# Kernel tuning notes

Hardware: AMD Instinct MI355X
Metric: run time of the kernel (lower is better)

The kernel has to match this reference:

```python
import jax, jax.numpy as jnp
import numpy as np

NUM_HEADER = 8
DIM_HIDDEN = 512
DIM_HEADER = DIM_HIDDEN // NUM_HEADER


def setup_inputs() -> dict:
    key = jax.random.key(0)
    ks = jax.random.split(key, 11)
    B, S, D = 2, 4096, DIM_HIDDEN
    scale = 1.0 / np.sqrt(D)
    inp = {
        "q": jax.random.normal(ks[0], (B, S, D), jnp.float32),
        "k": jax.random.normal(ks[1], (B, S, D), jnp.float32),
        "v": jax.random.normal(ks[2], (B, S, D), jnp.float32),
        # nn.Linear weights are [out, in]; y = x @ W.T + b
        "Wq": jax.random.normal(ks[3], (D, D), jnp.float32) * scale,
        "bq": jax.random.normal(ks[4], (D,), jnp.float32) * scale,
        "Wk": jax.random.normal(ks[5], (D, D), jnp.float32) * scale,
        "bk": jax.random.normal(ks[6], (D,), jnp.float32) * scale,
        "Wv": jax.random.normal(ks[7], (D, D), jnp.float32) * scale,
        "bv": jax.random.normal(ks[8], (D,), jnp.float32) * scale,
        "Wo": jax.random.normal(ks[9], (D, D), jnp.float32) * scale,
        "bo": jax.random.normal(ks[10], (D,), jnp.float32) * scale,
    }
    return inp


def reference(q, k, v, Wq, bq, Wk, bk, Wv, bv, Wo, bo):
    B = q.shape[0]
    H, dh = NUM_HEADER, DIM_HEADER

    def proj(x, W, b):
        # [B,S,D] -> [B,H,S,dh]
        y = jnp.einsum('bsd,ed->bse', x, W) + b
        return y.reshape(B, -1, H, dh).transpose(0, 2, 1, 3)

    qh = proj(q, Wq, bq)
    kh = proj(k, Wk, bk)
    vh = proj(v, Wv, bv)

    scores = jnp.einsum('bhqd,bhkd->bhqk', qh, kh) / jnp.sqrt(jnp.float32(dh))
    attn = jax.nn.softmax(scores, axis=-1)
    ctx = jnp.einsum('bhqk,bhkd->bhqd', attn, vh)
    concat = ctx.transpose(0, 2, 1, 3).reshape(B, -1, H * dh)
    return jnp.einsum('bsd,ed->bse', concat, Wo) + bo
```

## Files before the change

kernel.cpp:

```cpp
#include <hip/hip_runtime.h>
#include <hip/hip_bf16.h>

typedef __attribute__((ext_vector_type(8))) short short8;
typedef __attribute__((ext_vector_type(4))) float f32x4;
typedef __attribute__((ext_vector_type(16))) float f32x16;
typedef __attribute__((ext_vector_type(4))) float f4v;

#define SEQ 4096
#define NBH 16
#define SCALE_Q 0.18033688011112042f
#define CSHIFT 16.0f

#define MFMA16(a, b, c) __builtin_amdgcn_mfma_f32_16x16x32_bf16(a, b, c, 0, 0, 0)
#define MFMA32(a, b, c) __builtin_amdgcn_mfma_f32_32x32x16_bf16(a, b, c, 0, 0, 0)

__device__ __forceinline__ short f2bf(float f) {
  union { float f; unsigned u; } x; x.f = f;
  unsigned r = x.u + 0x7FFFu + ((x.u >> 16) & 1u);
  return (short)(r >> 16);
}

__device__ __forceinline__ unsigned cvt_pk_bf16(float lo, float hi) {
  unsigned r;
  asm("v_cvt_pk_bf16_f32 %0, %1, %2" : "=v"(r) : "v"(lo), "v"(hi));
  return r;
}

__device__ __forceinline__ short8 cvt8(const float* __restrict__ src) {
  f4v v0 = *(const f4v*)src;
  f4v v1 = *(const f4v*)(src + 4);
  union { unsigned u[4]; short8 s; } r;
  r.u[0] = cvt_pk_bf16(v0[0], v0[1]);
  r.u[1] = cvt_pk_bf16(v0[2], v0[3]);
  r.u[2] = cvt_pk_bf16(v1[0], v1[1]);
  r.u[3] = cvt_pk_bf16(v1[2], v1[3]);
  return r.s;
}

__device__ __forceinline__ void gll16(const void* g, void* l) {
  __builtin_amdgcn_global_load_lds(
      (const __attribute__((address_space(1))) void*)g,
      (__attribute__((address_space(3))) void*)l, 16, 0, 0);
}

__device__ __forceinline__ void pswap(unsigned& a, unsigned& b) {
  asm volatile("v_permlane32_swap_b32 %0, %1" : "+v"(a), "+v"(b));
}

__global__ __launch_bounds__(256) void cvt_w(
    const float* __restrict__ w0, const float* __restrict__ w1,
    const float* __restrict__ w2, const float* __restrict__ w3,
    short* __restrict__ dst)
{
  int i = blockIdx.x * 256 + threadIdx.x;
  int m = i >> 15;
  int off = (i & 32767) * 8;
  const float* s = (m == 0) ? w0 : (m == 1) ? w1 : (m == 2) ? w2 : w3;
  *(short8*)(dst + (size_t)m * 262144 + off) = cvt8(s + off);
}

template <int MODE>
__global__ __launch_bounds__(256) void gemm_bt(
    const float* __restrict__ Af, const short* __restrict__ Ab,
    const short* __restrict__ Wb, const float* __restrict__ bias,
    void* __restrict__ Cout)
{
  __shared__ __align__(16) char smemA[64 * 72 * 2];
  __shared__ __align__(16) char smemB[128 * 64 * 2];
  short (*As)[72] = (short(*)[72])smemA;
  const int t    = threadIdx.x;
  const int lane = t & 63;
  const int w    = t >> 6;
  const int g    = lane >> 4;
  const int q    = lane & 15;
  const int tile_n = blockIdx.x * 128;
  const int tile_m = blockIdx.y * 64;

  f32x4 acc[4][2];
#pragma unroll
  for (int mi = 0; mi < 4; ++mi)
#pragma unroll
    for (int ni = 0; ni < 2; ++ni)
#pragma unroll
      for (int j = 0; j < 4; ++j) acc[mi][ni][j] = 0.f;

  for (int k0 = 0; k0 < 512; k0 += 64) {
    __syncthreads();
    if (MODE != 3) {
#pragma unroll
      for (int it = 0; it < 2; ++it) {
        int i = it * 256 + t;
        int r = i >> 3, sg = i & 7;
        *(short8*)&As[r][sg * 8] =
            cvt8(Af + (size_t)(tile_m + r) * 512 + k0 + sg * 8);
      }
    } else {
#pragma unroll
      for (int it = 0; it < 2; ++it) {
        int i = it * 256 + t;
        int row = i >> 3, cg = i & 7;
        const char* gp = (const char*)Ab +
            ((size_t)(tile_m + row) * 512 + k0) * 2 + ((cg ^ (row & 7)) << 4);
        gll16(gp, smemA + (size_t)(it * 256 + (t & ~63)) * 16);
      }
    }
#pragma unroll
    for (int it = 0; it < 4; ++it) {
      int i = it * 256 + t;
      int row = i >> 3, cg = i & 7;
      const char* gp = (const char*)Wb +
          ((size_t)(tile_n + row) * 512 + k0) * 2 + ((cg ^ (row & 7)) << 4);
      gll16(gp, smemB + (size_t)(it * 256 + (t & ~63)) * 16);
    }
    __syncthreads();
#pragma unroll
    for (int kk = 0; kk < 2; ++kk) {
      short8 af[4], bfv[2];
#pragma unroll
      for (int mi = 0; mi < 4; ++mi) {
        int rA = mi * 16 + q;
        if (MODE != 3)
          af[mi] = *(const short8*)&As[rA][kk * 32 + g * 8];
        else
          af[mi] = *(const short8*)(smemA + rA * 128 +
                                    (((4 * kk + g) ^ (rA & 7)) << 4));
      }
#pragma unroll
      for (int ni = 0; ni < 2; ++ni) {
        int rB = w * 32 + ni * 16 + q;
        bfv[ni] = *(const short8*)(smemB + rB * 128 +
                                   (((4 * kk + g) ^ (rB & 7)) << 4));
      }
#pragma unroll
      for (int mi = 0; mi < 4; ++mi)
#pragma unroll
        for (int ni = 0; ni < 2; ++ni) {
          if (MODE == 2)
            acc[mi][ni] = MFMA16(bfv[ni], af[mi], acc[mi][ni]);
          else
            acc[mi][ni] = MFMA16(af[mi], bfv[ni], acc[mi][ni]);
        }
    }
  }

#pragma unroll
  for (int mi = 0; mi < 4; ++mi) {
#pragma unroll
    for (int ni = 0; ni < 2; ++ni) {
#pragma unroll
      for (int j = 0; j < 4; ++j) {
        if (MODE == 2) {
          int e = tile_n + w * 32 + ni * 16 + 4 * g + j;
          int srow = tile_m + mi * 16 + q;
          float val = acc[mi][ni][j] + bias[e];
          int b = srow >> 12, sl = srow & 4095;
          int h = e >> 6, d = e & 63;
          ((short*)Cout)[((size_t)((b * 8 + h) * 64 + d)) * SEQ + sl] = f2bf(val);
        } else {
          int m = tile_m + mi * 16 + g * 4 + j;
          int e = tile_n + w * 32 + ni * 16 + q;
          float val = acc[mi][ni][j] + bias[e];
          if (MODE == 0) val *= SCALE_Q;
          if (MODE == 3) {
            ((float*)Cout)[(size_t)m * 512 + e] = val;
          } else {
            int b = m >> 12, s = m & 4095;
            int h = e >> 6, d = e & 63;
            ((short*)Cout)[((size_t)(b * 8 + h) * SEQ + s) * 64 + d] = f2bf(val);
          }
        }
      }
    }
  }
}

template <int NSPLIT>
__global__ __launch_bounds__(256, 4) void attn_kernel(
    const short* __restrict__ Qh, const short* __restrict__ Kh,
    const short* __restrict__ Vt, short* __restrict__ ctx,
    float* __restrict__ Opart, float* __restrict__ lsum)
{
  __shared__ __align__(16) char smem[2][16384];
  const int t    = threadIdx.x;
  const int lane = t & 63;
  const int w    = t >> 6;
  const int l31  = lane & 31;
  const int hi   = lane >> 5;

  const int fid = blockIdx.x;
  int qt, bh, split;
  if (NSPLIT == 1) {
    int lid = (fid & 7) * 64 + (fid >> 3);
    qt = lid & 31; bh = lid >> 5; split = 0;
  } else {
    int lid = (fid & 7) * 128 + (fid >> 3);
    qt = lid & 31; split = (lid >> 5) & 1; bh = lid >> 6;
  }
  const int NT  = (SEQ / 64) / NSPLIT;
  const int kt0 = split * NT;

  const size_t kbase = (size_t)bh * SEQ * 64;
  const size_t vbase = (size_t)bh * 64 * SEQ;
  const int q0 = qt * 128 + w * 32;

  short8 qf[4];
#pragma unroll
  for (int m = 0; m < 4; ++m)
    qf[m] = *(const short8*)(Qh + kbase + (size_t)(q0 + l31) * 64 + m * 16 + hi * 8);

  f32x16 fz, fm;
#pragma unroll
  for (int r = 0; r < 16; ++r) { fz[r] = 0.f; fm[r] = -CSHIFT; }
  f32x16 acc0 = fz, acc1 = fz;
  float lrun = 0.f;

  const int rif  = lane >> 3;
  const int scol = ((lane & 7) ^ rif) * 16;
  const int xr   = (hi * 16) ^ ((lane & 7) << 4);

#define STAGE(buf, kt)                                                         \
  {                                                                            \
    _Pragma("unroll")                                                          \
    for (int i = 0; i < 4; ++i) {                                              \
      int c = w * 4 + i;                                                       \
      char* ldst = &smem[buf][c * 1024];                                       \
      if (c < 8) {                                                             \
        int row = c * 8 + rif;                                                 \
        const char* gp = (const char*)Kh +                                     \
            ((kbase + (size_t)((kt) * 64 + row) * 64) * 2 + scol);             \
        gll16(gp, ldst);                                                       \
      } else {                                                                 \
        int row = (c - 8) * 8 + rif;                                           \
        const char* gp = (const char*)Vt +                                     \
            ((vbase + (size_t)row * SEQ + (kt) * 64) * 2 + scol);              \
        gll16(gp, ldst);                                                       \
      }                                                                        \
    }                                                                          \
  }

  STAGE(0, kt0);
  int cur = 0;

  for (int it = 0; it < NT; ++it) {
    const int kt = kt0 + it;
    if (it < NT - 1) {
      STAGE(cur ^ 1, kt + 1);
      asm volatile("s_waitcnt vmcnt(4)" ::: "memory");
    } else {
      asm volatile("s_waitcnt vmcnt(0)" ::: "memory");
    }
    __builtin_amdgcn_sched_barrier(0);
    __builtin_amdgcn_s_barrier();
    __builtin_amdgcn_sched_barrier(0);

    const char* Kb = &smem[cur][0];
    const char* Vb = &smem[cur][8192];

    f32x16 s0, s1;
    {
      short8 k0 = *(const short8*)(Kb + (size_t)(l31) * 128 + ((32 * 0) ^ xr));
      short8 k1 = *(const short8*)(Kb + (size_t)(32 + l31) * 128 + ((32 * 0) ^ xr));
      __builtin_amdgcn_s_setprio(1);
      s0 = MFMA32(k0, qf[0], fm);
      s1 = MFMA32(k1, qf[0], fm);
      __builtin_amdgcn_s_setprio(0);
    }
#pragma unroll
    for (int m = 1; m < 4; ++m) {
      short8 k0 = *(const short8*)(Kb + (size_t)(l31) * 128 + ((32 * m) ^ xr));
      short8 k1 = *(const short8*)(Kb + (size_t)(32 + l31) * 128 + ((32 * m) ^ xr));
      __builtin_amdgcn_s_setprio(1);
      s0 = MFMA32(k0, qf[m], s0);
      s1 = MFMA32(k1, qf[m], s1);
      __builtin_amdgcn_s_setprio(0);
    }

#pragma unroll
    for (int r = 0; r < 16; ++r) s0[r] = __builtin_amdgcn_exp2f(s0[r]);
    float rs0;
    {
      float b_[8];
#pragma unroll
      for (int r = 0; r < 8; ++r) b_[r] = s0[r] + s0[r + 8];
#pragma unroll
      for (int r = 0; r < 4; ++r) b_[r] += b_[r + 4];
      rs0 = (b_[0] + b_[1]) + (b_[2] + b_[3]);
    }
    union { unsigned u[4]; short8 v; } A0c, A1c;
    {
      unsigned p0 = cvt_pk_bf16(s0[0], s0[1]);
      unsigned p1 = cvt_pk_bf16(s0[2], s0[3]);
      unsigned p2 = cvt_pk_bf16(s0[4], s0[5]);
      unsigned p3 = cvt_pk_bf16(s0[6], s0[7]);
      unsigned p4 = cvt_pk_bf16(s0[8], s0[9]);
      unsigned p5 = cvt_pk_bf16(s0[10], s0[11]);
      unsigned p6 = cvt_pk_bf16(s0[12], s0[13]);
      unsigned p7 = cvt_pk_bf16(s0[14], s0[15]);
      pswap(p0, p2); pswap(p1, p3); pswap(p4, p6); pswap(p5, p7);
      A0c.u[0] = p0; A0c.u[1] = p1; A0c.u[2] = p2; A0c.u[3] = p3;
      A1c.u[0] = p4; A1c.u[1] = p5; A1c.u[2] = p6; A1c.u[3] = p7;
    }
#pragma unroll
    for (int h2 = 0; h2 < 2; ++h2) {
      short8 pa = h2 ? A1c.v : A0c.v;
      short8 vf0 = *(const short8*)(Vb + (size_t)(l31) * 128 + ((32 * h2) ^ xr));
      short8 vf1 = *(const short8*)(Vb + (size_t)(32 + l31) * 128 + ((32 * h2) ^ xr));
      __builtin_amdgcn_s_setprio(1);
      acc0 = MFMA32(pa, vf0, acc0);
      acc1 = MFMA32(pa, vf1, acc1);
      __builtin_amdgcn_s_setprio(0);
    }

#pragma unroll
    for (int r = 0; r < 16; ++r) s1[r] = __builtin_amdgcn_exp2f(s1[r]);
    float rs1;
    {
      float b_[8];
#pragma unroll
      for (int r = 0; r < 8; ++r) b_[r] = s1[r] + s1[r + 8];
#pragma unroll
      for (int r = 0; r < 4; ++r) b_[r] += b_[r + 4];
      rs1 = (b_[0] + b_[1]) + (b_[2] + b_[3]);
    }
    {
      unsigned p0 = cvt_pk_bf16(s1[0], s1[1]);
      unsigned p1 = cvt_pk_bf16(s1[2], s1[3]);
      unsigned p2 = cvt_pk_bf16(s1[4], s1[5]);
      unsigned p3 = cvt_pk_bf16(s1[6], s1[7]);
      unsigned p4 = cvt_pk_bf16(s1[8], s1[9]);
      unsigned p5 = cvt_pk_bf16(s1[10], s1[11]);
      unsigned p6 = cvt_pk_bf16(s1[12], s1[13]);
      unsigned p7 = cvt_pk_bf16(s1[14], s1[15]);
      pswap(p0, p2); pswap(p1, p3); pswap(p4, p6); pswap(p5, p7);
      A0c.u[0] = p0; A0c.u[1] = p1; A0c.u[2] = p2; A0c.u[3] = p3;
      A1c.u[0] = p4; A1c.u[1] = p5; A1c.u[2] = p6; A1c.u[3] = p7;
    }
#pragma unroll
    for (int h2 = 0; h2 < 2; ++h2) {
      short8 pa = h2 ? A1c.v : A0c.v;
      short8 vf0 = *(const short8*)(Vb + (size_t)(l31) * 128 + ((64 + 32 * h2) ^ xr));
      short8 vf1 = *(const short8*)(Vb + (size_t)(32 + l31) * 128 + ((64 + 32 * h2) ^ xr));
      __builtin_amdgcn_s_setprio(1);
      acc0 = MFMA32(pa, vf0, acc0);
      acc1 = MFMA32(pa, vf1, acc1);
      __builtin_amdgcn_s_setprio(0);
    }

    float rs = rs0 + rs1;
    rs += __shfl_xor(rs, 32);
    lrun += rs;

    __builtin_amdgcn_sched_barrier(0);
    __builtin_amdgcn_s_barrier();
    __builtin_amdgcn_sched_barrier(0);
    cur ^= 1;
  }

  if (NSPLIT == 1) {
    const int b = bh >> 3, hh = bh & 7;
    const float inv = 1.0f / lrun;
#pragma unroll
    for (int r = 0; r < 16; ++r) {
      int ql = (r & 3) + 8 * (r >> 2) + 4 * hi;
      float iv = __shfl(inv, ql);
      int qrow = q0 + ql;
      size_t off = ((size_t)(b * SEQ + qrow)) * 512 + hh * 64 + l31;
      ctx[off]      = f2bf(acc0[r] * iv);
      ctx[off + 32] = f2bf(acc1[r] * iv);
    }
  } else {
    float* Ob = Opart + (((size_t)(split * NBH + bh) * SEQ + q0)) * 64;
#pragma unroll
    for (int r = 0; r < 16; ++r) {
      int ql = (r & 3) + 8 * (r >> 2) + 4 * hi;
      Ob[(size_t)ql * 64 + l31]      = acc0[r];
      Ob[(size_t)ql * 64 + l31 + 32] = acc1[r];
    }
    if (hi == 0)
      lsum[(size_t)(split * NBH + bh) * SEQ + q0 + l31] = lrun;
  }
}

__global__ __launch_bounds__(256) void merge_kernel(
    const float* __restrict__ Opart, const float* __restrict__ lsum,
    short* __restrict__ ctx)
{
  int idx = blockIdx.x * 256 + threadIdx.x;
  int dg = idx & 7;
  int qq = (idx >> 3) & 4095;
  int bh = idx >> 15;
  size_t r0 = (size_t)bh * SEQ + qq;
  size_t r1 = (size_t)(NBH + bh) * SEQ + qq;
  float inv = 1.0f / (lsum[r0] + lsum[r1]);
  const float* o0 = Opart + r0 * 64 + dg * 8;
  const float* o1 = Opart + r1 * 64 + dg * 8;
  f4v a0 = *(const f4v*)o0, a1 = *(const f4v*)(o0 + 4);
  f4v b0 = *(const f4v*)o1, b1 = *(const f4v*)(o1 + 4);
  float v[8];
#pragma unroll
  for (int j = 0; j < 4; ++j) v[j] = (a0[j] + b0[j]) * inv;
#pragma unroll
  for (int j = 0; j < 4; ++j) v[4 + j] = (a1[j] + b1[j]) * inv;
  union { unsigned u[4]; short8 s; } r;
  r.u[0] = cvt_pk_bf16(v[0], v[1]);
  r.u[1] = cvt_pk_bf16(v[2], v[3]);
  r.u[2] = cvt_pk_bf16(v[4], v[5]);
  r.u[3] = cvt_pk_bf16(v[6], v[7]);
  *(short8*)(ctx + ((size_t)(bh >> 3) * SEQ + qq) * 512 + (bh & 7) * 64 + dg * 8) = r.s;
}

extern "C" void kernel_launch(void* const* d_in, const int* in_sizes, int n_in,
                              void* d_out, int out_size, void* d_ws, size_t ws_size,
                              hipStream_t stream) {
  const float* q  = (const float*)d_in[0];
  const float* k  = (const float*)d_in[1];
  const float* v  = (const float*)d_in[2];
  const float* Wq = (const float*)d_in[3];
  const float* bq = (const float*)d_in[4];
  const float* Wk = (const float*)d_in[5];
  const float* bk = (const float*)d_in[6];
  const float* Wv = (const float*)d_in[7];
  const float* bv = (const float*)d_in[8];
  const float* Wo = (const float*)d_in[9];
  const float* bo = (const float*)d_in[10];

  const size_t NELT = (size_t)NBH * SEQ * 64;
  short* Qh  = (short*)d_ws;
  short* Kh  = Qh + NELT;
  short* Vt  = Kh + NELT;
  short* ctx = Vt + NELT;
  short* Wb  = ctx + NELT;
  float* Opart = (float*)(Wb + 4 * 262144);
  float* lsum  = Opart + 2 * (size_t)NBH * SEQ * 64;
  const char* ws_end = (const char*)(lsum + 2 * (size_t)NBH * SEQ);
  const bool split2 = ws_size >= (size_t)(ws_end - (const char*)d_ws);

  dim3 tb(256);
  cvt_w<<<dim3(512), tb, 0, stream>>>(Wq, Wk, Wv, Wo, Wb);

  dim3 gb(4, 128);
  gemm_bt<0><<<gb, tb, 0, stream>>>(q, nullptr, Wb,          bq, (void*)Qh);
  gemm_bt<1><<<gb, tb, 0, stream>>>(k, nullptr, Wb + 262144, bk, (void*)Kh);
  gemm_bt<2><<<gb, tb, 0, stream>>>(v, nullptr, Wb + 524288, bv, (void*)Vt);
  if (split2) {
    attn_kernel<2><<<dim3(1024), tb, 0, stream>>>(Qh, Kh, Vt, ctx, Opart, lsum);
    merge_kernel<<<dim3(NBH * SEQ * 8 / 256), tb, 0, stream>>>(Opart, lsum, ctx);
  } else {
    attn_kernel<1><<<dim3(512), tb, 0, stream>>>(Qh, Kh, Vt, ctx, Opart, lsum);
  }
  gemm_bt<3><<<gb, tb, 0, stream>>>(nullptr, ctx, Wb + 786432, bo, d_out);
}
```

Before: 178.7 us.

## Restructure attention loop into barrier-phased load/MFMA/softmax stages for wave ping-pong

Reorders the flash-attention inner loop so each iteration first issues the next tile prefetch and batches all K fragment reads from LDS. It then separates the QK MFMA, V fragment loads plus exp/convert, and PV MFMA phases with workgroup barriers. The goal is to keep waves in lockstep phases so MFMA and VALU/LDS work interleave across waves, hiding LDS latency. It adds several extra s_barriers per tile and increases register pressure from holding K and V fragments, and the global-load wait moves to the end of the iteration.

After: 342.8 us. 1.92x slower.

```diff
diff --git a/kernel.cpp b/kernel.cpp
--- a/kernel.cpp
+++ b/kernel.cpp
@@ -46,6 +46,11 @@
 __device__ __forceinline__ void pswap(unsigned& a, unsigned& b) {
   asm volatile("v_permlane32_swap_b32 %0, %1" : "+v"(a), "+v"(b));
 }
+
+#define SBAR()                              \
+  __builtin_amdgcn_sched_barrier(0);        \
+  __builtin_amdgcn_s_barrier();             \
+  __builtin_amdgcn_sched_barrier(0)
 
 __global__ __launch_bounds__(256) void cvt_w(
     const float* __restrict__ w0, const float* __restrict__ w1,
@@ -239,42 +244,39 @@
   }
 
   STAGE(0, kt0);
+  asm volatile("s_waitcnt vmcnt(0)" ::: "memory");
+  SBAR();
   int cur = 0;
 
   for (int it = 0; it < NT; ++it) {
     const int kt = kt0 + it;
-    if (it < NT - 1) {
-      STAGE(cur ^ 1, kt + 1);
-      asm volatile("s_waitcnt vmcnt(4)" ::: "memory");
-    } else {
-      asm volatile("s_waitcnt vmcnt(0)" ::: "memory");
-    }
-    __builtin_amdgcn_sched_barrier(0);
-    __builtin_amdgcn_s_barrier();
-    __builtin_amdgcn_sched_barrier(0);
-
     const char* Kb = &smem[cur][0];
     const char* Vb = &smem[cur][8192];
 
+    if (it < NT - 1) STAGE(cur ^ 1, kt + 1);
+    short8 kf0[4], kf1[4];
+#pragma unroll
+    for (int m = 0; m < 4; ++m) {
+      kf0[m] = *(const short8*)(Kb + (size_t)(l31) * 128 + ((32 * m) ^ xr));
+      kf1[m] = *(const short8*)(Kb + (size_t)(32 + l31) * 128 + ((32 * m) ^ xr));
+    }
+    SBAR();
     f32x16 s0, s1;
-    {
-      short8 k0 = *(const short8*)(Kb + (size_t)(l31) * 128 + ((32 * 0) ^ xr));
-      short8 k1 = *(const short8*)(Kb + (size_t)(32 + l31) * 128 + ((32 * 0) ^ xr));
-      __builtin_amdgcn_s_setprio(1);
-      s0 = MFMA32(k0, qf[0], fm);
-      s1 = MFMA32(k1, qf[0], fm);
-      __builtin_amdgcn_s_setprio(0);
-    }
+    __builtin_amdgcn_s_setprio(1);
+    s0 = MFMA32(kf0[0], qf[0], fm);
+    s1 = MFMA32(kf1[0], qf[0], fm);
 #pragma unroll
     for (int m = 1; m < 4; ++m) {
-      short8 k0 = *(const short8*)(Kb + (size_t)(l31) * 128 + ((32 * m) ^ xr));
-      short8 k1 = *(const short8*)(Kb + (size_t)(32 + l31) * 128 + ((32 * m) ^ xr));
-      __builtin_amdgcn_s_setprio(1);
-      s0 = MFMA32(k0, qf[m], s0);
-      s1 = MFMA32(k1, qf[m], s1);
-      __builtin_amdgcn_s_setprio(0);
-    }
-
+      s0 = MFMA32(kf0[m], qf[m], s0);
+      s1 = MFMA32(kf1[m], qf[m], s1);
+    }
+    __builtin_amdgcn_s_setprio(0);
+    SBAR();
+
+    short8 v00 = *(const short8*)(Vb + (size_t)(l31) * 128 + ((0) ^ xr));
+    short8 v01 = *(const short8*)(Vb + (size_t)(32 + l31) * 128 + ((0) ^ xr));
+    short8 v02 = *(const short8*)(Vb + (size_t)(l31) * 128 + ((32) ^ xr));
+    short8 v03 = *(const short8*)(Vb + (size_t)(32 + l31) * 128 + ((32) ^ xr));
 #pragma unroll
     for (int r = 0; r < 16; ++r) s0[r] = __builtin_amdgcn_exp2f(s0[r]);
     float rs0;
@@ -300,17 +302,19 @@
       A0c.u[0] = p0; A0c.u[1] = p1; A0c.u[2] = p2; A0c.u[3] = p3;
       A1c.u[0] = p4; A1c.u[1] = p5; A1c.u[2] = p6; A1c.u[3] = p7;
     }
-#pragma unroll
-    for (int h2 = 0; h2 < 2; ++h2) {
-      short8 pa = h2 ? A1c.v : A0c.v;
-      short8 vf0 = *(const short8*)(Vb + (size_t)(l31) * 128 + ((32 * h2) ^ xr));
-      short8 vf1 = *(const short8*)(Vb + (size_t)(32 + l31) * 128 + ((32 * h2) ^ xr));
-      __builtin_amdgcn_s_setprio(1);
-      acc0 = MFMA32(pa, vf0, acc0);
-      acc1 = MFMA32(pa, vf1, acc1);
-      __builtin_amdgcn_s_setprio(0);
-    }
-
+    SBAR();
+    __builtin_amdgcn_s_setprio(1);
+    acc0 = MFMA32(A0c.v, v00, acc0);
+    acc1 = MFMA32(A0c.v, v01, acc1);
+    acc0 = MFMA32(A1c.v, v02, acc0);
+    acc1 = MFMA32(A1c.v, v03, acc1);
+    __builtin_amdgcn_s_setprio(0);
+    SBAR();
+
+    short8 v10 = *(const short8*)(Vb + (size_t)(l31) * 128 + ((64) ^ xr));
+    short8 v11 = *(const short8*)(Vb + (size_t)(32 + l31) * 128 + ((64) ^ xr));
+    short8 v12 = *(const short8*)(Vb + (size_t)(l31) * 128 + ((96) ^ xr));
+    short8 v13 = *(const short8*)(Vb + (size_t)(32 + l31) * 128 + ((96) ^ xr));
 #pragma unroll
     for (int r = 0; r < 16; ++r) s1[r] = __builtin_amdgcn_exp2f(s1[r]);
     float rs1;
@@ -335,24 +339,20 @@
       A0c.u[0] = p0; A0c.u[1] = p1; A0c.u[2] = p2; A0c.u[3] = p3;
       A1c.u[0] = p4; A1c.u[1] = p5; A1c.u[2] = p6; A1c.u[3] = p7;
     }
-#pragma unroll
-    for (int h2 = 0; h2 < 2; ++h2) {
-      short8 pa = h2 ? A1c.v : A0c.v;
-      short8 vf0 = *(const short8*)(Vb + (size_t)(l31) * 128 + ((64 + 32 * h2) ^ xr));
-      short8 vf1 = *(const short8*)(Vb + (size_t)(32 + l31) * 128 + ((64 + 32 * h2) ^ xr));
-      __builtin_amdgcn_s_setprio(1);
-      acc0 = MFMA32(pa, vf0, acc0);
-      acc1 = MFMA32(pa, vf1, acc1);
-      __builtin_amdgcn_s_setprio(0);
-    }
+    SBAR();
+    __builtin_amdgcn_s_setprio(1);
+    acc0 = MFMA32(A0c.v, v10, acc0);
+    acc1 = MFMA32(A0c.v, v11, acc1);
+    acc0 = MFMA32(A1c.v, v12, acc0);
+    acc1 = MFMA32(A1c.v, v13, acc1);
+    __builtin_amdgcn_s_setprio(0);
 
     float rs = rs0 + rs1;
     rs += __shfl_xor(rs, 32);
     lrun += rs;
 
-    __builtin_amdgcn_sched_barrier(0);
-    __builtin_amdgcn_s_barrier();
-    __builtin_amdgcn_sched_barrier(0);
+    asm volatile("s_waitcnt vmcnt(0)" ::: "memory");
+    SBAR();
     cur ^= 1;
   }
 
```

## Fuse split-attention merge into output projection GEMM A-tile loading

Applied to the files above, without the earlier changes.

Removes the separate merge kernel and instead combines the two split partial outputs and normalizes them while loading the A tile of the output projection GEMM. This saves a kernel launch and the bf16 ctx write/read round trip. In exchange, each of the four column blocks re-reads the fp32 partials and recomputes the merge. The constant shift fed into the score MFMA accumulator is also dropped.

New measurement: 160.9 us. 1.11x faster.

```diff
diff --git a/kernel.cpp b/kernel.cpp
--- a/kernel.cpp
+++ b/kernel.cpp
@@ -9,7 +9,6 @@
 #define SEQ 4096
 #define NBH 16
 #define SCALE_Q 0.18033688011112042f
-#define CSHIFT 16.0f
 
 #define MFMA16(a, b, c) __builtin_amdgcn_mfma_f32_16x16x32_bf16(a, b, c, 0, 0, 0)
 #define MFMA32(a, b, c) __builtin_amdgcn_mfma_f32_32x32x16_bf16(a, b, c, 0, 0, 0)
@@ -46,6 +45,11 @@
 __device__ __forceinline__ void pswap(unsigned& a, unsigned& b) {
   asm volatile("v_permlane32_swap_b32 %0, %1" : "+v"(a), "+v"(b));
 }
+
+#define SBAR()                              \
+  __builtin_amdgcn_sched_barrier(0);        \
+  __builtin_amdgcn_s_barrier();             \
+  __builtin_amdgcn_sched_barrier(0)
 
 __global__ __launch_bounds__(256) void cvt_w(
     const float* __restrict__ w0, const float* __restrict__ w1,
@@ -63,6 +67,7 @@
 __global__ __launch_bounds__(256) void gemm_bt(
     const float* __restrict__ Af, const short* __restrict__ Ab,
     const short* __restrict__ Wb, const float* __restrict__ bias,
+    const float* __restrict__ Opart, const float* __restrict__ lsum,
     void* __restrict__ Cout)
 {
   __shared__ __align__(16) char smemA[64 * 72 * 2];
@@ -86,7 +91,7 @@
 
   for (int k0 = 0; k0 < 512; k0 += 64) {
     __syncthreads();
-    if (MODE != 3) {
+    if (MODE <= 2) {
 #pragma unroll
       for (int it = 0; it < 2; ++it) {
         int i = it * 256 + t;
@@ -94,7 +99,7 @@
         *(short8*)&As[r][sg * 8] =
             cvt8(Af + (size_t)(tile_m + r) * 512 + k0 + sg * 8);
       }
-    } else {
+    } else if (MODE == 3) {
 #pragma unroll
       for (int it = 0; it < 2; ++it) {
         int i = it * 256 + t;
@@ -103,6 +108,33 @@
             ((size_t)(tile_m + row) * 512 + k0) * 2 + ((cg ^ (row & 7)) << 4);
         gll16(gp, smemA + (size_t)(it * 256 + (t & ~63)) * 16);
       }
+    } else {
+#pragma unroll
+      for (int it = 0; it < 2; ++it) {
+        int i = it * 256 + t;
+        int row = i >> 3, cg = i & 7;
+        int cgs = cg ^ (row & 7);
+        int m = tile_m + row;
+        int b = m >> 12, s = m & 4095;
+        int h = k0 >> 6;
+        size_t g0 = (size_t)(b * 8 + h) * SEQ + s;
+        float inv = 1.0f / (lsum[g0] + lsum[g0 + (size_t)NBH * SEQ]);
+        const float* o0 = Opart + g0 * 64 + cgs * 8;
+        const float* o1 = Opart + (g0 + (size_t)NBH * SEQ) * 64 + cgs * 8;
+        f4v a0 = *(const f4v*)o0, a1 = *(const f4v*)(o0 + 4);
+        f4v b0 = *(const f4v*)o1, b1 = *(const f4v*)(o1 + 4);
+        float vv[8];
+#pragma unroll
+        for (int j = 0; j < 4; ++j) vv[j] = (a0[j] + b0[j]) * inv;
+#pragma unroll
+        for (int j = 0; j < 4; ++j) vv[4 + j] = (a1[j] + b1[j]) * inv;
+        union { unsigned u[4]; short8 s8; } r;
+        r.u[0] = cvt_pk_bf16(vv[0], vv[1]);
+        r.u[1] = cvt_pk_bf16(vv[2], vv[3]);
+        r.u[2] = cvt_pk_bf16(vv[4], vv[5]);
+        r.u[3] = cvt_pk_bf16(vv[6], vv[7]);
+        *(short8*)(smemA + (size_t)i * 16) = r.s8;
+      }
     }
 #pragma unroll
     for (int it = 0; it < 4; ++it) {
@@ -119,7 +151,7 @@
 #pragma unroll
       for (int mi = 0; mi < 4; ++mi) {
         int rA = mi * 16 + q;
-        if (MODE != 3)
+        if (MODE <= 2)
           af[mi] = *(const short8*)&As[rA][kk * 32 + g * 8];
         else
           af[mi] = *(const short8*)(smemA + rA * 128 +
@@ -161,7 +193,7 @@
           int e = tile_n + w * 32 + ni * 16 + q;
           float val = acc[mi][ni][j] + bias[e];
           if (MODE == 0) val *= SCALE_Q;
-          if (MODE == 3) {
+          if (MODE >= 3) {
             ((float*)Cout)[(size_t)m * 512 + e] = val;
           } else {
             int b = m >> 12, s = m & 4095;
@@ -208,9 +240,9 @@
   for (int m = 0; m < 4; ++m)
     qf[m] = *(const short8*)(Qh + kbase + (size_t)(q0 + l31) * 64 + m * 16 + hi * 8);
 
-  f32x16 fz, fm;
-#pragma unroll
-  for (int r = 0; r < 16; ++r) { fz[r] = 0.f; fm[r] = -CSHIFT; }
+  f32x16 fz;
+#pragma unroll
+  for (int r = 0; r < 16; ++r) fz[r] = 0.f;
   f32x16 acc0 = fz, acc1 = fz;
   float lrun = 0.f;
 
@@ -249,9 +281,7 @@
     } else {
       asm volatile("s_waitcnt vmcnt(0)" ::: "memory");
     }
-    __builtin_amdgcn_sched_barrier(0);
-    __builtin_amdgcn_s_barrier();
-    __builtin_amdgcn_sched_barrier(0);
+    SBAR();
 
     const char* Kb = &smem[cur][0];
     const char* Vb = &smem[cur][8192];
@@ -261,8 +291,8 @@
       short8 k0 = *(const short8*)(Kb + (size_t)(l31) * 128 + ((32 * 0) ^ xr));
       short8 k1 = *(const short8*)(Kb + (size_t)(32 + l31) * 128 + ((32 * 0) ^ xr));
       __builtin_amdgcn_s_setprio(1);
-      s0 = MFMA32(k0, qf[0], fm);
-      s1 = MFMA32(k1, qf[0], fm);
+      s0 = MFMA32(k0, qf[0], fz);
+      s1 = MFMA32(k1, qf[0], fz);
       __builtin_amdgcn_s_setprio(0);
     }
 #pragma unroll
@@ -350,9 +380,7 @@
     rs += __shfl_xor(rs, 32);
     lrun += rs;
 
-    __builtin_amdgcn_sched_barrier(0);
-    __builtin_amdgcn_s_barrier();
-    __builtin_amdgcn_sched_barrier(0);
+    SBAR();
     cur ^= 1;
   }
 
@@ -379,34 +407,6 @@
     if (hi == 0)
       lsum[(size_t)(split * NBH + bh) * SEQ + q0 + l31] = lrun;
   }
-}
-
-__global__ __launch_bounds__(256) void merge_kernel(
-    const float* __restrict__ Opart, const float* __restrict__ lsum,
-    short* __restrict__ ctx)
-{
-  int idx = blockIdx.x * 256 + threadIdx.x;
-  int dg = idx & 7;
-  int qq = (idx >> 3) & 4095;
-  int bh = idx >> 15;
-  size_t r0 = (size_t)bh * SEQ + qq;
-  size_t r1 = (size_t)(NBH + bh) * SEQ + qq;
-  float inv = 1.0f / (lsum[r0] + lsum[r1]);
-  const float* o0 = Opart + r0 * 64 + dg * 8;
-  const float* o1 = Opart + r1 * 64 + dg * 8;
-  f4v a0 = *(const f4v*)o0, a1 = *(const f4v*)(o0 + 4);
-  f4v b0 = *(const f4v*)o1, b1 = *(const f4v*)(o1 + 4);
-  float v[8];
-#pragma unroll
-  for (int j = 0; j < 4; ++j) v[j] = (a0[j] + b0[j]) * inv;
-#pragma unroll
-  for (int j = 0; j < 4; ++j) v[4 + j] = (a1[j] + b1[j]) * inv;
-  union { unsigned u[4]; short8 s; } r;
-  r.u[0] = cvt_pk_bf16(v[0], v[1]);
-  r.u[1] = cvt_pk_bf16(v[2], v[3]);
-  r.u[2] = cvt_pk_bf16(v[4], v[5]);
-  r.u[3] = cvt_pk_bf16(v[6], v[7]);
-  *(short8*)(ctx + ((size_t)(bh >> 3) * SEQ + qq) * 512 + (bh & 7) * 64 + dg * 8) = r.s;
 }
 
 extern "C" void kernel_launch(void* const* d_in, const int* in_sizes, int n_in,
@@ -439,14 +439,14 @@
   cvt_w<<<dim3(512), tb, 0, stream>>>(Wq, Wk, Wv, Wo, Wb);
 
   dim3 gb(4, 128);
-  gemm_bt<0><<<gb, tb, 0, stream>>>(q, nullptr, Wb,          bq, (void*)Qh);
-  gemm_bt<1><<<gb, tb, 0, stream>>>(k, nullptr, Wb + 262144, bk, (void*)Kh);
-  gemm_bt<2><<<gb, tb, 0, stream>>>(v, nullptr, Wb + 524288, bv, (void*)Vt);
+  gemm_bt<0><<<gb, tb, 0, stream>>>(q, nullptr, Wb,          bq, nullptr, nullptr, (void*)Qh);
+  gemm_bt<1><<<gb, tb, 0, stream>>>(k, nullptr, Wb + 262144, bk, nullptr, nullptr, (void*)Kh);
+  gemm_bt<2><<<gb, tb, 0, stream>>>(v, nullptr, Wb + 524288, bv, nullptr, nullptr, (void*)Vt);
   if (split2) {
     attn_kernel<2><<<dim3(1024), tb, 0, stream>>>(Qh, Kh, Vt, ctx, Opart, lsum);
-    merge_kernel<<<dim3(NBH * SEQ * 8 / 256), tb, 0, stream>>>(Opart, lsum, ctx);
+    gemm_bt<4><<<gb, tb, 0, stream>>>(nullptr, nullptr, Wb + 786432, bo, Opart, lsum, d_out);
   } else {
     attn_kernel<1><<<dim3(512), tb, 0, stream>>>(Qh, Kh, Vt, ctx, Opart, lsum);
-  }
-  gemm_bt<3><<<gb, tb, 0, stream>>>(nullptr, ctx, Wb + 786432, bo, d_out);
-}
+    gemm_bt<3><<<gb, tb, 0, stream>>>(nullptr, ctx, Wb + 786432, bo, nullptr, nullptr, d_out);
+  }
+}
```
